# Performance work log

Measured on AMD Instinct MI355X. Metric: run time of the kernel, lower is better.

## Reference

```python
import jax, jax.numpy as jnp
import numpy as np

DIM = 1024
DFF = 4096
B, L = 4, 4096


def _lin_init(key, din, dout):
    k1, k2 = jax.random.split(key)
    bound = 1.0 / np.sqrt(din)
    w = jax.random.uniform(k1, (din, dout), jnp.float32, -bound, bound)
    b = jax.random.uniform(k2, (dout,), jnp.float32, -bound, bound)
    return w, b


def setup_inputs() -> dict:
    key = jax.random.key(0)
    ks = jax.random.split(key, 12)
    x = jax.random.normal(ks[0], (B, L, DIM), jnp.float32)
    hidden = jax.random.normal(ks[1], (B, DIM), jnp.float32)
    w_ln_z, b_ln_z = _lin_init(ks[2], DIM, DIM)
    w_dt, b_dt = _lin_init(ks[3], DIM, DIM)
    w_y, b_y = _lin_init(ks[4], DIM, DIM)
    w_yg, b_yg = _lin_init(ks[5], DIM, DIM)
    w_ff, b_ff = _lin_init(ks[6], DIM, DFF)
    w_ffg, b_ffg = _lin_init(ks[7], DIM, DFF)
    w_ffo, b_ffo = _lin_init(ks[8], DFF, DIM)
    g_sio = jnp.ones((DIM,), jnp.float32)
    g_ffn = jnp.ones((DIM,), jnp.float32)
    return dict(x=x, hidden=hidden, w_ln_z=w_ln_z, b_ln_z=b_ln_z, w_dt=w_dt,
                b_dt=b_dt, w_y=w_y, b_y=b_y, w_yg=w_yg, b_yg=b_yg,
                w_ff=w_ff, b_ff=b_ff, w_ffg=w_ffg, b_ffg=b_ffg,
                w_ffo=w_ffo, b_ffo=b_ffo, g_sio=g_sio, g_ffn=g_ffn)


def _rmsnorm(x, g, eps=1e-6):
    return x * jax.lax.rsqrt(jnp.mean(x * x, axis=-1, keepdims=True) + eps) * g


def reference(x, hidden, w_ln_z, b_ln_z, w_dt, b_dt, w_y, b_y, w_yg, b_yg,
              w_ff, b_ff, w_ffg, b_ffg, w_ffo, b_ffo, g_sio, g_ffn):
    silu = jax.nn.silu
    sp = jax.nn.softplus
    # --- SioConv branch ---
    residual = x
    xn = _rmsnorm(x, g_sio)
    dt = xn @ w_dt + b_dt
    ln_z = -sp(-(xn @ w_ln_z + b_ln_z))
    ln_da = -sp(-dt)           # log sigmoid(dt)
    ln_o_da = -sp(dt)          # log sigmoid(-dt)
    ln_o_da_cumsum = jnp.cumsum(ln_o_da, axis=1)
    lcse = jax.lax.cumlogsumexp(ln_z + ln_da - ln_o_da_cumsum, axis=1)
    h_inner = jnp.exp(lcse + ln_o_da_cumsum)                 # [B,L,D]
    h_cross = jnp.exp(ln_o_da_cumsum) * hidden[:, None, :]   # [B,L,D]
    h = h_inner + h_cross
    y = (h @ w_y + b_y) * silu(xn @ w_yg + b_yg)
    x = y + residual
    # --- FFN branch ---
    residual = x
    xn = _rmsnorm(x, g_ffn)
    ff = ((xn @ w_ff + b_ff) * silu(xn @ w_ffg + b_ffg)) @ w_ffo + b_ffo
    x = ff + residual
    return (x, h)
```

## Files before the change

kernel.cpp:

```cpp
#include <hip/hip_runtime.h>
#include <cstdint>
#include <cstddef>

using u16 = unsigned short;
using bf16x8 = __attribute__((ext_vector_type(8))) short;
using f32x4  = __attribute__((ext_vector_type(4))) float;

__device__ __forceinline__ u16 f2bf(float f) {
  unsigned u = __float_as_uint(f);
  u += 0x7fffu + ((u >> 16) & 1u);
  return (u16)(u >> 16);
}
__device__ __forceinline__ float bf2f(u16 h) {
  return __uint_as_float(((unsigned)h) << 16);
}

__device__ __forceinline__ void gload_lds16(const void* g, void* l) {
  auto gp = reinterpret_cast<const __attribute__((address_space(1))) char*>(
      reinterpret_cast<uintptr_t>(g));
  auto lp = reinterpret_cast<__attribute__((address_space(3))) char*>(
      reinterpret_cast<uintptr_t>(l));
  __builtin_amdgcn_global_load_lds(gp, lp, 16, 0, 0);
}

__global__ __launch_bounds__(256) void transpose_to_bf16(
    const float* __restrict__ W, u16* __restrict__ WT, int din, int dout) {
  __shared__ float tile[32][33];
  const int j0 = blockIdx.x * 32;
  const int i0 = blockIdx.y * 32;
  const int tx = threadIdx.x & 31;
  const int ty = threadIdx.x >> 5;
#pragma unroll
  for (int k = 0; k < 32; k += 8)
    tile[ty + k][tx] = W[(size_t)(i0 + ty + k) * dout + (j0 + tx)];
  __syncthreads();
#pragma unroll
  for (int k = 0; k < 32; k += 8)
    WT[(size_t)(j0 + ty + k) * din + (i0 + tx)] = f2bf(tile[tx][ty + k]);
}

__global__ __launch_bounds__(256) void rmsnorm_kernel(
    const float* __restrict__ x, const float* __restrict__ g, u16* __restrict__ xn) {
  const int row = blockIdx.x;
  const float4 v = ((const float4*)(x + (size_t)row * 1024))[threadIdx.x];
  float ss = v.x * v.x + v.y * v.y + v.z * v.z + v.w * v.w;
#pragma unroll
  for (int off = 32; off > 0; off >>= 1) ss += __shfl_down(ss, off, 64);
  __shared__ float red[4];
  if ((threadIdx.x & 63) == 0) red[threadIdx.x >> 6] = ss;
  __syncthreads();
  const float rs = rsqrtf((red[0] + red[1] + red[2] + red[3]) * (1.f / 1024.f) + 1e-6f);
  const float4 gv = ((const float4*)g)[threadIdx.x];
  ushort4 o;
  o.x = f2bf(v.x * rs * gv.x);
  o.y = f2bf(v.y * rs * gv.y);
  o.z = f2bf(v.z * rs * gv.z);
  o.w = f2bf(v.w * rs * gv.w);
  ((ushort4*)(xn + (size_t)row * 1024))[threadIdx.x] = o;
}

__global__ __launch_bounds__(256) void scan_pass1(
    const u16* __restrict__ dt, const u16* __restrict__ lnz,
    float* __restrict__ P, float* __restrict__ S) {
  const int blk = blockIdx.x;
  const int dblk = blk & 3;
  const int chunk = (blk >> 2) & 63;
  const int b = blk >> 8;
  const int d = dblk * 256 + threadIdx.x;
  const size_t base = ((size_t)b * 4096 + (size_t)chunk * 64) * 1024 + d;
  float p = 1.f, s = 0.f;
#pragma unroll 8
  for (int l = 0; l < 64; ++l) {
    const float dtv = bf2f(dt[base + (size_t)l * 1024]);
    const float zv = bf2f(lnz[base + (size_t)l * 1024]);
    const float a = 1.f / (1.f + __expf(dtv));
    const float zs = 1.f / (1.f + __expf(-zv));
    const float in = (1.f - a) * zs;
    p *= a;
    s = a * s + in;
  }
  const size_t o = ((size_t)b * 64 + chunk) * 1024 + d;
  P[o] = p;
  S[o] = s;
}

__global__ __launch_bounds__(256) void scan_pass2(
    const float* __restrict__ P, const float* __restrict__ S,
    const float* __restrict__ hidden, float* __restrict__ hin) {
  const int idx = blockIdx.x * 256 + threadIdx.x;
  const int b = idx >> 10, d = idx & 1023;
  float h = hidden[idx];
#pragma unroll 8
  for (int c = 0; c < 64; ++c) {
    const size_t o = ((size_t)b * 64 + c) * 1024 + d;
    hin[o] = h;
    h = P[o] * h + S[o];
  }
}

__global__ __launch_bounds__(256) void scan_pass3(
    const u16* __restrict__ dt, const u16* __restrict__ lnz,
    const float* __restrict__ hin, float* __restrict__ h_out, u16* __restrict__ hbf) {
  const int blk = blockIdx.x;
  const int dblk = blk & 3;
  const int chunk = (blk >> 2) & 63;
  const int b = blk >> 8;
  const int d = dblk * 256 + threadIdx.x;
  const size_t base = ((size_t)b * 4096 + (size_t)chunk * 64) * 1024 + d;
  float h = hin[((size_t)b * 64 + chunk) * 1024 + d];
#pragma unroll 4
  for (int l = 0; l < 64; ++l) {
    const float dtv = bf2f(dt[base + (size_t)l * 1024]);
    const float zv = bf2f(lnz[base + (size_t)l * 1024]);
    const float a = 1.f / (1.f + __expf(dtv));
    const float zs = 1.f / (1.f + __expf(-zv));
    h = a * h + (1.f - a) * zs;
    h_out[base + (size_t)l * 1024] = h;
    hbf[base + (size_t)l * 1024] = f2bf(h);
  }
}

template <int EPI>
__global__ __launch_bounds__(512, 4) void gemm_pair(
    const u16* __restrict__ A, const u16* __restrict__ B1, const u16* __restrict__ B2,
    const float* __restrict__ biasA, const float* __restrict__ biasB,
    const u16* __restrict__ gate, const float* __restrict__ resid,
    float* __restrict__ outF, u16* __restrict__ outH,
    u16* __restrict__ outH2, u16* __restrict__ outH3,
    int ntx, int N, int K) {
  constexpr int SLOT = 16384;
  constexpr bool GATED = (EPI == 3);
  const int tid = threadIdx.x;
  const int lane = tid & 63;
  const int wid = tid >> 6;
  const int wrow = wid >> 1;
  const int wcol = wid & 1;
  const int whalf = wrow >> 1;
  const int wsub  = wrow & 1;

  const int nwg = gridDim.x;
  int id = blockIdx.x;
  id = (id & 7) * (nwg >> 3) + (id >> 3);
  const int m0 = (id / ntx) * 256;
  const int n0 = (id % ntx) * (GATED ? 64 : 128);

  __shared__ __align__(16) char lds[5 * SLOT];

  f32x4 acc1[4][2], acc2[4][2];
#pragma unroll
  for (int m = 0; m < 4; ++m)
#pragma unroll
    for (int n = 0; n < 2; ++n) {
      acc1[m][n] = (f32x4){0.f, 0.f, 0.f, 0.f};
      acc2[m][n] = (f32x4){0.f, 0.f, 0.f, 0.f};
    }

  bf16x8 aR[2];
  bf16x8 b1R[2][2], b2R[2][2];

  int aOff0, bOff0;
  {
    const int lq = (lane >> 4) << 4;
    const int ha = wsub * 64 + (lane & 15);
    aOff0 = ha * 128 + (lq ^ ((ha & 7) << 4));
    const int hb = wcol * 32 + (lane & 15);
    bOff0 = hb * 128 + (lq ^ ((hb & 7) << 4));
  }

  const int row0 = tid >> 3;
  const int kb0  = ((tid & 7) * 16) ^ ((row0 & 7) << 4);
  const size_t dRow = (size_t)128 * K;
  const char* pA0 = (const char*)A + (size_t)(m0 + row0) * K * 2 + kb0;
  const char* pA1 = pA0 + (size_t)256 * K;
  const char* pB1 = (const char*)B1 + (size_t)(n0 + row0) * K * 2 + kb0;
  const char* pB2 = (const char*)B2 +
                    (size_t)((GATED ? n0 : n0 + 64) + row0) * K * 2 + kb0;
  const int ldst = tid * 16;

#define STAGEA(PTR, SB)                                                       \
  {                                                                           \
    gload_lds16(PTR, lds + (SB) + ldst);                                      \
    gload_lds16(PTR + dRow, lds + (SB) + ldst + 8192);                        \
    PTR += 128;                                                               \
  }
#define STAGEB(PTR, SB, OFF)                                                  \
  {                                                                           \
    gload_lds16(PTR, lds + (SB) + (OFF) + ldst);                              \
    PTR += 128;                                                               \
  }

#define READA(SAB, Q)                                                         \
  {                                                                           \
    const int _o = aOff0 + (Q) * 2048;                                        \
    aR[0] = *(const bf16x8*)(lds + (SAB) + _o);                               \
    aR[1] = *(const bf16x8*)(lds + (SAB) + (_o ^ 64));                        \
  }

#define READBD(SBB)                                                           \
  _Pragma("unroll") for (int n = 0; n < 2; ++n) {                             \
    const int _o = bOff0 + n * 2048;                                          \
    b1R[n][0] = *(const bf16x8*)(lds + (SBB) + _o);                           \
    b1R[n][1] = *(const bf16x8*)(lds + (SBB) + (_o ^ 64));                    \
    b2R[n][0] = *(const bf16x8*)(lds + (SBB) + 8192 + _o);                    \
    b2R[n][1] = *(const bf16x8*)(lds + (SBB) + 8192 + (_o ^ 64));             \
  }

#define MMAD(Q)                                                               \
  __builtin_amdgcn_s_setprio(1);                                              \
  _Pragma("unroll") for (int n = 0; n < 2; ++n)                               \
  _Pragma("unroll") for (int k = 0; k < 2; ++k) {                             \
    acc1[Q][n] = __builtin_amdgcn_mfma_f32_16x16x32_bf16(                     \
        aR[k], b1R[n][k], acc1[Q][n], 0, 0, 0);                               \
    acc2[Q][n] = __builtin_amdgcn_mfma_f32_16x16x32_bf16(                     \
        aR[k], b2R[n][k], acc2[Q][n], 0, 0, 0);                               \
  }                                                                           \
  __builtin_amdgcn_s_setprio(0);

  const int NT = K >> 6;

  STAGEB(pB1, 0 * SLOT, 0);
  STAGEB(pB2, 0 * SLOT, 8192);
  STAGEA(pA0, 1 * SLOT);
  STAGEA(pA1, 2 * SLOT);
  asm volatile("s_waitcnt vmcnt(0)" ::: "memory");
  __builtin_amdgcn_s_barrier();

  int iB = 0;

  for (int t = 0; t < NT; ++t) {
    int ib1 = iB + 1 + whalf; if (ib1 >= 5) ib1 -= 5;
    const int sAb = __builtin_amdgcn_readfirstlane(ib1 * SLOT);
    const int sBb = __builtin_amdgcn_readfirstlane(iB * SLOT);
    int i0s = iB + 3; if (i0s >= 5) i0s -= 5;
    int i1s = iB + 4; if (i1s >= 5) i1s -= 5;
    const int s0 = i0s * SLOT, s1 = i1s * SLOT, s2 = iB * SLOT;
    const bool st = (t < NT - 1);
    READBD(sBb);
    READA(sAb, 0);
    if (st) {
      STAGEB(pB1, s0, 0);
      STAGEB(pB2, s0, 8192);
    }
    MMAD(0);
    READA(sAb, 1);
    if (st) STAGEA(pA0, s1);
    MMAD(1);
    READA(sAb, 2);
    MMAD(2);
    __builtin_amdgcn_s_barrier();
    READA(sAb, 3);
    if (st) STAGEA(pA1, s2);
    MMAD(3);
    asm volatile("s_waitcnt vmcnt(0)" ::: "memory");
    __builtin_amdgcn_s_barrier();
    iB += 3; if (iB >= 5) iB -= 5;
  }

#pragma unroll
  for (int m = 0; m < 4; ++m) {
#pragma unroll
    for (int n = 0; n < 2; ++n) {
#pragma unroll
      for (int j = 0; j < 4; ++j) {
        const int row = m0 + wrow * 64 + m * 16 + ((lane >> 4) << 2) + j;
        if constexpr (GATED) {
          const int col = n0 + wcol * 32 + n * 16 + (lane & 15);
          const float v1 = acc1[m][n][j] + biasA[col];
          const float v2 = acc2[m][n][j] + biasB[col];
          outH[(size_t)row * N + col] = f2bf(v1 * (v2 / (1.f + __expf(-v2))));
        } else {
#pragma unroll
          for (int s = 0; s < 2; ++s) {
            const int col = n0 + s * 64 + wcol * 32 + n * 16 + (lane & 15);
            const float v = (s == 0 ? acc1[m][n][j] : acc2[m][n][j]) + biasA[col];
            if constexpr (EPI == 5) {
              const int rg = col >> 10;
              const size_t o = (size_t)row * 1024 + (col & 1023);
              if (rg == 0) outH[o] = f2bf(v);
              else if (rg == 1) outH2[o] = f2bf(v);
              else outH3[o] = f2bf(v);
            } else {
              const size_t o = (size_t)row * N + col;
              if constexpr (EPI == 2) {
                const float gt = bf2f(gate[o]);
                outF[o] = v * (gt / (1.f + __expf(-gt))) + resid[o];
              } else if constexpr (EPI == 4) {
                outF[o] = v + outF[o];
              }
            }
          }
        }
      }
    }
  }
#undef STAGEA
#undef STAGEB
#undef READA
#undef READBD
#undef MMAD
}

extern "C" void kernel_launch(void* const* d_in, const int* in_sizes, int n_in,
                              void* d_out, int out_size, void* d_ws, size_t ws_size,
                              hipStream_t stream) {
  const float* x      = (const float*)d_in[0];
  const float* hidden = (const float*)d_in[1];
  const float* w_ln_z = (const float*)d_in[2];
  const float* b_ln_z = (const float*)d_in[3];
  const float* w_dt   = (const float*)d_in[4];
  const float* b_dt   = (const float*)d_in[5];
  const float* w_y    = (const float*)d_in[6];
  const float* b_y    = (const float*)d_in[7];
  const float* w_yg   = (const float*)d_in[8];
  const float* b_yg   = (const float*)d_in[9];
  const float* w_ff   = (const float*)d_in[10];
  const float* b_ff   = (const float*)d_in[11];
  const float* w_ffg  = (const float*)d_in[12];
  const float* b_ffg  = (const float*)d_in[13];
  const float* w_ffo  = (const float*)d_in[14];
  const float* b_ffo  = (const float*)d_in[15];
  const float* g_sio  = (const float*)d_in[16];
  const float* g_ffn  = (const float*)d_in[17];

  char* ws = (char*)d_ws;
  const size_t MB = 1ull << 20;
  u16*   WT_cat = (u16*)(ws + 0 * MB);
  u16*   WT_y   = (u16*)(ws + 8 * MB);
  u16*   WT_ff  = (u16*)(ws + 10 * MB);
  u16*   WT_ffg = (u16*)(ws + 18 * MB);
  u16*   WT_ffo = (u16*)(ws + 26 * MB);
  float* b_cat  = (float*)(ws + 34 * MB);
  u16*   xn     = (u16*)(ws + 36 * MB);
  u16*   dt16   = (u16*)(ws + 68 * MB);
  u16*   lnzb   = (u16*)(ws + 100 * MB);
  u16*   ygb    = (u16*)(ws + 132 * MB);
  u16*   hbf    = (u16*)(ws + 164 * MB);
  float* Pc     = (float*)(ws + 196 * MB);
  float* Sc     = (float*)(ws + 197 * MB);
  float* hin    = (float*)(ws + 198 * MB);
  u16*   gs     = (u16*)(ws + 68 * MB);

  float* x_out = (float*)d_out;
  float* h_out = (float*)d_out + (size_t)4 * 4096 * 1024;

  const int M = 16384, D = 1024, F = 4096;
  const dim3 tb(256);

  transpose_to_bf16<<<dim3(32, 32), tb, 0, stream>>>(w_dt, WT_cat, D, D);
  transpose_to_bf16<<<dim3(32, 32), tb, 0, stream>>>(w_ln_z, WT_cat + 1024 * 1024, D, D);
  transpose_to_bf16<<<dim3(32, 32), tb, 0, stream>>>(w_yg, WT_cat + 2 * 1024 * 1024, D, D);
  transpose_to_bf16<<<dim3(32, 32), tb, 0, stream>>>(w_y, WT_y, D, D);
  transpose_to_bf16<<<dim3(128, 32), tb, 0, stream>>>(w_ff, WT_ff, D, F);
  transpose_to_bf16<<<dim3(128, 32), tb, 0, stream>>>(w_ffg, WT_ffg, D, F);
  transpose_to_bf16<<<dim3(32, 128), tb, 0, stream>>>(w_ffo, WT_ffo, F, D);
  (void)hipMemcpyAsync(b_cat, b_dt, D * 4, hipMemcpyDeviceToDevice, stream);
  (void)hipMemcpyAsync(b_cat + 1024, b_ln_z, D * 4, hipMemcpyDeviceToDevice, stream);
  (void)hipMemcpyAsync(b_cat + 2048, b_yg, D * 4, hipMemcpyDeviceToDevice, stream);

  rmsnorm_kernel<<<M, tb, 0, stream>>>(x, g_sio, xn);

  gemm_pair<5><<<dim3(64 * 24), 512, 0, stream>>>(
      xn, WT_cat, WT_cat, b_cat, nullptr, nullptr, nullptr,
      nullptr, dt16, lnzb, ygb, 24, 3072, D);

  scan_pass1<<<1024, tb, 0, stream>>>(dt16, lnzb, Pc, Sc);
  scan_pass2<<<16, tb, 0, stream>>>(Pc, Sc, hidden, hin);
  scan_pass3<<<1024, tb, 0, stream>>>(dt16, lnzb, hin, h_out, hbf);

  gemm_pair<2><<<dim3(64 * 8), 512, 0, stream>>>(
      hbf, WT_y, WT_y, b_y, nullptr, ygb, x,
      x_out, nullptr, nullptr, nullptr, 8, D, D);

  rmsnorm_kernel<<<M, tb, 0, stream>>>(x_out, g_ffn, xn);

  gemm_pair<3><<<dim3(64 * 64), 512, 0, stream>>>(
      xn, WT_ff, WT_ffg, b_ff, b_ffg, nullptr, nullptr,
      nullptr, gs, nullptr, nullptr, 64, F, D);

  gemm_pair<4><<<dim3(64 * 8), 512, 0, stream>>>(
      gs, WT_ffo, WT_ffo, b_ffo, nullptr, nullptr, nullptr,
      x_out, nullptr, nullptr, nullptr, 8, D, F);
}
```

Measured before the change: 716.8 us.

## Parallelize chunk-carry scan with wave shuffles and batch weight-transpose launches

Scan pass 2 previously ran 16 blocks that walked 64 chunks serially per channel. It now uses a warp-level Hillstrom-style shuffle scan across the 64 chunks, with the P/S/hin layout changed to channel-major so each wave reads contiguous values. The seven weight transposes are merged into three multi-slice launches, and the three bias memcpys become one small kernel, cutting launch overhead. Pass 1 and pass 3 writes and reads are now strided by 64 floats, which may reduce coalescing on those small tensors.

```diff
diff --git a/kernel.cpp b/kernel.cpp
--- a/kernel.cpp
+++ b/kernel.cpp
@@ -23,8 +23,16 @@
   __builtin_amdgcn_global_load_lds(gp, lp, 16, 0, 0);
 }
 
-__global__ __launch_bounds__(256) void transpose_to_bf16(
-    const float* __restrict__ W, u16* __restrict__ WT, int din, int dout) {
+__global__ __launch_bounds__(256) void transpose4(
+    const float* W0, const float* W1, const float* W2, const float* W3,
+    u16* T0, u16* T1, u16* T2, u16* T3, int din, int dout) {
+  const float* W; u16* T;
+  switch (blockIdx.z) {
+    case 0: W = W0; T = T0; break;
+    case 1: W = W1; T = T1; break;
+    case 2: W = W2; T = T2; break;
+    default: W = W3; T = T3; break;
+  }
   __shared__ float tile[32][33];
   const int j0 = blockIdx.x * 32;
   const int i0 = blockIdx.y * 32;
@@ -36,7 +44,14 @@
   __syncthreads();
 #pragma unroll
   for (int k = 0; k < 32; k += 8)
-    WT[(size_t)(j0 + ty + k) * din + (i0 + tx)] = f2bf(tile[tx][ty + k]);
+    T[(size_t)(j0 + ty + k) * din + (i0 + tx)] = f2bf(tile[tx][ty + k]);
+}
+
+__global__ __launch_bounds__(256) void concat_bias(
+    const float* __restrict__ a, const float* __restrict__ b,
+    const float* __restrict__ c, float* __restrict__ o) {
+  const int i = blockIdx.x * 256 + threadIdx.x;
+  o[i] = (i < 1024) ? a[i] : (i < 2048 ? b[i - 1024] : c[i - 2048]);
 }
 
 __global__ __launch_bounds__(256) void rmsnorm_kernel(
@@ -79,7 +94,7 @@
     p *= a;
     s = a * s + in;
   }
-  const size_t o = ((size_t)b * 64 + chunk) * 1024 + d;
+  const size_t o = ((size_t)b * 1024 + d) * 64 + chunk;
   P[o] = p;
   S[o] = s;
 }
@@ -87,15 +102,21 @@
 __global__ __launch_bounds__(256) void scan_pass2(
     const float* __restrict__ P, const float* __restrict__ S,
     const float* __restrict__ hidden, float* __restrict__ hin) {
-  const int idx = blockIdx.x * 256 + threadIdx.x;
-  const int b = idx >> 10, d = idx & 1023;
-  float h = hidden[idx];
-#pragma unroll 8
-  for (int c = 0; c < 64; ++c) {
-    const size_t o = ((size_t)b * 64 + c) * 1024 + d;
-    hin[o] = h;
-    h = P[o] * h + S[o];
-  }
+  const int ch = blockIdx.x * 4 + (threadIdx.x >> 6);
+  const int lane = threadIdx.x & 63;
+  const size_t base = (size_t)ch * 64;
+  float p = P[base + lane];
+  float s = S[base + lane];
+#pragma unroll
+  for (int off = 1; off < 64; off <<= 1) {
+    const float pp = __shfl_up(p, off, 64);
+    const float sp = __shfl_up(s, off, 64);
+    if (lane >= off) { s = p * sp + s; p = p * pp; }
+  }
+  float pe = __shfl_up(p, 1, 64);
+  float se = __shfl_up(s, 1, 64);
+  if (lane == 0) { pe = 1.f; se = 0.f; }
+  hin[base + lane] = pe * hidden[ch] + se;
 }
 
 __global__ __launch_bounds__(256) void scan_pass3(
@@ -107,7 +128,7 @@
   const int b = blk >> 8;
   const int d = dblk * 256 + threadIdx.x;
   const size_t base = ((size_t)b * 4096 + (size_t)chunk * 64) * 1024 + d;
-  float h = hin[((size_t)b * 64 + chunk) * 1024 + d];
+  float h = hin[((size_t)b * 1024 + d) * 64 + chunk];
 #pragma unroll 4
   for (int l = 0; l < 64; ++l) {
     const float dtv = bf2f(dt[base + (size_t)l * 1024]);
@@ -346,16 +367,14 @@
   const int M = 16384, D = 1024, F = 4096;
   const dim3 tb(256);
 
-  transpose_to_bf16<<<dim3(32, 32), tb, 0, stream>>>(w_dt, WT_cat, D, D);
-  transpose_to_bf16<<<dim3(32, 32), tb, 0, stream>>>(w_ln_z, WT_cat + 1024 * 1024, D, D);
-  transpose_to_bf16<<<dim3(32, 32), tb, 0, stream>>>(w_yg, WT_cat + 2 * 1024 * 1024, D, D);
-  transpose_to_bf16<<<dim3(32, 32), tb, 0, stream>>>(w_y, WT_y, D, D);
-  transpose_to_bf16<<<dim3(128, 32), tb, 0, stream>>>(w_ff, WT_ff, D, F);
-  transpose_to_bf16<<<dim3(128, 32), tb, 0, stream>>>(w_ffg, WT_ffg, D, F);
-  transpose_to_bf16<<<dim3(32, 128), tb, 0, stream>>>(w_ffo, WT_ffo, F, D);
-  (void)hipMemcpyAsync(b_cat, b_dt, D * 4, hipMemcpyDeviceToDevice, stream);
-  (void)hipMemcpyAsync(b_cat + 1024, b_ln_z, D * 4, hipMemcpyDeviceToDevice, stream);
-  (void)hipMemcpyAsync(b_cat + 2048, b_yg, D * 4, hipMemcpyDeviceToDevice, stream);
+  transpose4<<<dim3(32, 32, 4), tb, 0, stream>>>(
+      w_dt, w_ln_z, w_yg, w_y,
+      WT_cat, WT_cat + 1024 * 1024, WT_cat + 2 * 1024 * 1024, WT_y, D, D);
+  transpose4<<<dim3(128, 32, 2), tb, 0, stream>>>(
+      w_ff, w_ffg, w_ff, w_ffg, WT_ff, WT_ffg, WT_ff, WT_ffg, D, F);
+  transpose4<<<dim3(32, 128, 1), tb, 0, stream>>>(
+      w_ffo, w_ffo, w_ffo, w_ffo, WT_ffo, WT_ffo, WT_ffo, WT_ffo, F, D);
+  concat_bias<<<12, tb, 0, stream>>>(b_dt, b_ln_z, b_yg, b_cat);
 
   rmsnorm_kernel<<<M, tb, 0, stream>>>(x, g_sio, xn);
 
@@ -364,7 +383,7 @@
       nullptr, dt16, lnzb, ygb, 24, 3072, D);
 
   scan_pass1<<<1024, tb, 0, stream>>>(dt16, lnzb, Pc, Sc);
-  scan_pass2<<<16, tb, 0, stream>>>(Pc, Sc, hidden, hin);
+  scan_pass2<<<1024, tb, 0, stream>>>(Pc, Sc, hidden, hin);
   scan_pass3<<<1024, tb, 0, stream>>>(dt16, lnzb, hin, h_out, hbf);
 
   gemm_pair<2><<<dim3(64 * 8), 512, 0, stream>>>(
```

New measurement: 701.7 us. -2.1%, faster.
